# Kernel optimization log

Measured on AMD Instinct MI355X. Metric: run time of the kernel, lower is better.

Reference implementation:

```python
import jax, jax.numpy as jnp
import numpy as np

B, S, D = 1, 2048, 2048
H, HD = 32, 64            # num_heads, head_dim = hidden/num_heads
CS, TOPK = 256, 4         # moba_chunk_size, moba_topk
ROPE_BASE = 10000.0
EPS = 1e-6


def setup_inputs() -> dict:
    key = jax.random.key(0)
    ks = jax.random.split(key, 8)
    w = lambda k, shape: jax.random.normal(k, shape, dtype=jnp.float32) * 0.02
    return {
        "hidden_states": jax.random.normal(ks[0], (B, S, D), dtype=jnp.float32),
        "Wq": w(ks[1], (D, D)),
        "Wk": w(ks[2], (D, D)),
        "Wv": w(ks[3], (D, D)),
        "Wo": w(ks[4], (D, D)),
        "Wg1": w(ks[5], (D, HD)),
        "Wg2": w(ks[6], (HD, D)),
        "o_norm_w": jnp.ones((HD,), dtype=jnp.float32),
    }


def _rope(x):
    # x: [B,S,H,HD]; non-interleaved half-rotation rotary over full head_dim
    s = x.shape[1]
    half = HD // 2
    inv = 1.0 / (ROPE_BASE ** (jnp.arange(half, dtype=jnp.float32) / half))
    freqs = jnp.arange(s, dtype=jnp.float32)[:, None] * inv[None, :]      # [S, half]
    cos = jnp.cos(freqs)[None, :, None, :]
    sin = jnp.sin(freqs)[None, :, None, :]
    x1, x2 = x[..., :half], x[..., half:]
    return jnp.concatenate([x1 * cos - x2 * sin, x2 * cos + x1 * sin], axis=-1)


def _moba_attn_single(q, k, v):
    # q,k,v: [S,H,HD]  (one varlen sequence)
    s = q.shape[0]
    n = s // CS                                  # number of KV chunks
    scale = HD ** -0.5
    # mean-pooled key per chunk -> gate logits
    kg = k.reshape(n, CS, H, HD).mean(axis=1)                    # [N,H,HD]
    gate = jnp.einsum('shd,nhd->hsn', q, kg)                     # [H,S,N]
    pos_chunk = jnp.arange(s) // CS                              # [S]
    n_idx = jnp.arange(n)
    is_self = pos_chunk[:, None] == n_idx[None, :]               # [S,N]
    not_past = pos_chunk[:, None] <= n_idx[None, :]              # self or future
    gate = jnp.where(not_past[None], -jnp.inf, gate)             # only strictly-past chunks selectable
    gate = jnp.where(is_self[None], jnp.inf, gate)               # self chunk always attended
    kk = min(TOPK, n)
    tv, ti = jax.lax.top_k(gate, kk)                             # [H,S,kk], sorted desc
    thr = tv[..., -1:]                                           # min of top-k
    need = gate >= thr
    idx_mask = jax.nn.one_hot(ti, n, dtype=jnp.bool_).any(axis=-2)  # [H,S,N]
    need = need & idx_mask                                       # selected chunks per (h, query)
    # expand chunk selection to per-key mask and add causal mask
    allow = need[:, :, pos_chunk]                                # [H,S,S]
    causal = jnp.arange(s)[None, :] <= jnp.arange(s)[:, None]    # [S,S]
    mask = allow & causal[None]
    scores = jnp.einsum('shd,thd->hst', q, k) * scale            # [H,S,S]
    p = jax.nn.softmax(jnp.where(mask, scores, -jnp.inf), axis=-1)
    return jnp.einsum('hst,thd->shd', p, v)                      # [S,H,HD]


def reference(hidden_states, Wq, Wk, Wv, Wo, Wg1, Wg2, o_norm_w):
    x = hidden_states
    q = (x @ Wq).reshape(B, S, H, HD)
    k = (x @ Wk).reshape(B, S, H, HD)
    v = (x @ Wv).reshape(B, S, H, HD)
    q, k = _rope(q), _rope(k)
    o = jax.vmap(_moba_attn_single)(q, k, v)                     # [B,S,H,HD]
    # FusedRMSNormGated(sigmoid): rmsnorm(o) * weight * sigmoid(g)
    g = ((x @ Wg1) @ Wg2).reshape(B, S, H, HD)
    var = jnp.mean(o * o, axis=-1, keepdims=True)
    o = o * jax.lax.rsqrt(var + EPS) * o_norm_w
    o = o * jax.nn.sigmoid(g)
    return o.reshape(B, S, D) @ Wo
```

## Files before the change

kernel.cpp:

```cpp
#include <hip/hip_runtime.h>
#include <hip/hip_bf16.h>
#include <math.h>

#define S_LEN 2048
#define D_DIM 2048
#define NH 32
#define HD 64
#define CS 256
#define NCH 8

typedef __attribute__((ext_vector_type(8))) short bf16x8;
typedef __attribute__((ext_vector_type(4))) short bf16x4;
typedef __attribute__((ext_vector_type(4))) float f32x4;

__device__ __forceinline__ unsigned short f2bf(float f) {
  unsigned int u = __builtin_bit_cast(unsigned int, f);
  unsigned int r = (u + 0x7fffu + ((u >> 16) & 1u)) >> 16;
  return (unsigned short)r;
}
__device__ __forceinline__ float bf2f(unsigned short b) {
  unsigned int u = ((unsigned int)b) << 16;
  return __builtin_bit_cast(float, u);
}

__device__ __forceinline__ f32x4 mfma16(bf16x4 a, bf16x4 b, f32x4 c) {
#if __has_builtin(__builtin_amdgcn_mfma_f32_16x16x16_bf16)
  return __builtin_amdgcn_mfma_f32_16x16x16_bf16(a, b, c, 0, 0, 0);
#elif __has_builtin(__builtin_amdgcn_mfma_f32_16x16x16bf16_1k)
  return __builtin_amdgcn_mfma_f32_16x16x16bf16_1k(a, b, c, 0, 0, 0);
#else
  asm("v_mfma_f32_16x16x16_bf16 %0, %1, %2, %0" : "+v"(c) : "v"(a), "v"(b));
  return c;
#endif
}

__device__ __forceinline__ void gload16(const void* gp, void* lp) {
  __builtin_amdgcn_global_load_lds(
      (const __attribute__((address_space(1))) unsigned int*)gp,
      (__attribute__((address_space(3))) unsigned int*)lp, 16, 0, 0);
}

struct QKVG {
  const unsigned short* xh;
  const unsigned short* xl;
  const unsigned short* wh[4];
  const unsigned short* wl[4];
  float* C[4];
  int np[4];
};

__global__ __launch_bounds__(256) void gemm_qkvg(QKVG g) {
  __shared__ __align__(16) unsigned short Als[128 * 64];
  __shared__ __align__(16) unsigned short Bls[128 * 64];
  const int tid = threadIdx.x;
  const int wid = tid >> 6, lane = tid & 63;
  const int l15 = lane & 15, l4 = lane >> 4;
  const int wr = wid >> 1, wc = wid & 1;
  const int K = D_DIM, N = D_DIM;

  const int bid = blockIdx.x;
  const int xcd = bid & 7;
  const int local = bid >> 3;
  const int c = local >> 6;
  const int idx = local & 63;
  const int out = (xcd & 1) + 2 * c;
  const int grp = xcd >> 1;
  const int row0 = (idx >> 2) << 7;
  const int col0 = ((grp << 2) + (idx & 3)) << 7;

  f32x4 acc[4][4];
#pragma unroll
  for (int m = 0; m < 4; ++m)
#pragma unroll
    for (int n = 0; n < 4; ++n) acc[m][n] = (f32x4){0.f, 0.f, 0.f, 0.f};

  const int np = g.np[out];
  for (int p = 0; p < np; ++p) {
    const unsigned short* Ap = (p == 2) ? g.xl : g.xh;
    const unsigned short* Bp = (p == 1) ? g.wl[out] : g.wh[out];
    for (int kt = 0; kt < K; kt += 64) {
      __syncthreads();
#pragma unroll
      for (int i = 0; i < 4; ++i) {
        const int Lb = i * 4096 + wid * 1024;
        const int L = Lb + lane * 16;
        const int row = L >> 7;
        const int s = (L >> 4) & 7;
        const int cofs = (s ^ (row & 7)) << 3;
        gload16(Ap + (size_t)(row0 + row) * K + kt + cofs, (char*)Als + Lb);
        gload16(Bp + (size_t)(col0 + row) * K + kt + cofs, (char*)Bls + Lb);
      }
      asm volatile("s_waitcnt vmcnt(0)" ::: "memory");
      __syncthreads();
#pragma unroll
      for (int ks = 0; ks < 2; ++ks) {
        bf16x8 af[4], bfr[4];
#pragma unroll
        for (int m = 0; m < 4; ++m) {
          int row = wr * 64 + m * 16 + l15;
          int s = (ks * 4 + l4) ^ (row & 7);
          af[m] = *reinterpret_cast<const bf16x8*>(&Als[row * 64 + s * 8]);
        }
#pragma unroll
        for (int n = 0; n < 4; ++n) {
          int col = wc * 64 + n * 16 + l15;
          int s = (ks * 4 + l4) ^ (col & 7);
          bfr[n] = *reinterpret_cast<const bf16x8*>(&Bls[col * 64 + s * 8]);
        }
#pragma unroll
        for (int m = 0; m < 4; ++m)
#pragma unroll
          for (int n = 0; n < 4; ++n)
            acc[m][n] = __builtin_amdgcn_mfma_f32_16x16x32_bf16(af[m], bfr[n], acc[m][n], 0, 0, 0);
      }
    }
  }

  float* C = g.C[out];
#pragma unroll
  for (int m = 0; m < 4; ++m)
#pragma unroll
    for (int n = 0; n < 4; ++n)
#pragma unroll
      for (int r = 0; r < 4; ++r)
        C[(size_t)(row0 + wr * 64 + m * 16 + l4 * 4 + r) * N + col0 + wc * 64 + n * 16 + l15] =
            acc[m][n][r];
}

struct G3 {
  const unsigned short* A[3];
  const unsigned short* B[3];
  int np;
};

__global__ __launch_bounds__(256) void gemm_bt(G3 g, float* __restrict__ C,
                                               int M, int N, int K) {
  __shared__ __align__(16) unsigned short Als[64 * 64];
  __shared__ __align__(16) unsigned short Bls[128 * 64];
  const int tid = threadIdx.x;
  const int wid = tid >> 6, lane = tid & 63;
  const int l15 = lane & 15, l4 = lane >> 4;
  const int wr = wid >> 1, wc = wid & 1;
  const int nbx = N >> 7;
  int bid = blockIdx.x;
  const int nwg = gridDim.x;
  if ((nwg & 7) == 0) {
    int q = nwg >> 3;
    bid = (bid & 7) * q + (bid >> 3);
  }
  const int row0 = (bid / nbx) << 6;
  const int col0 = (bid % nbx) << 7;

  f32x4 acc[2][4];
#pragma unroll
  for (int m = 0; m < 2; ++m)
#pragma unroll
    for (int n = 0; n < 4; ++n) acc[m][n] = (f32x4){0.f, 0.f, 0.f, 0.f};

  for (int p = 0; p < g.np; ++p) {
    const unsigned short* Ap = g.A[p];
    const unsigned short* Bp = g.B[p];
    for (int kt = 0; kt < K; kt += 64) {
      __syncthreads();
#pragma unroll
      for (int i = 0; i < 2; ++i) {
        const int Lb = i * 4096 + wid * 1024;
        const int L = Lb + lane * 16;
        const int row = L >> 7;
        const int s = (L >> 4) & 7;
        const int cofs = (s ^ (row & 7)) << 3;
        gload16(Ap + (size_t)(row0 + row) * K + kt + cofs, (char*)Als + Lb);
      }
#pragma unroll
      for (int i = 0; i < 4; ++i) {
        const int Lb = i * 4096 + wid * 1024;
        const int L = Lb + lane * 16;
        const int row = L >> 7;
        const int s = (L >> 4) & 7;
        const int cofs = (s ^ (row & 7)) << 3;
        gload16(Bp + (size_t)(col0 + row) * K + kt + cofs, (char*)Bls + Lb);
      }
      asm volatile("s_waitcnt vmcnt(0)" ::: "memory");
      __syncthreads();
#pragma unroll
      for (int ks = 0; ks < 2; ++ks) {
        bf16x8 af[2], bfr[4];
#pragma unroll
        for (int m = 0; m < 2; ++m) {
          int row = wr * 32 + m * 16 + l15;
          int s = (ks * 4 + l4) ^ (row & 7);
          af[m] = *reinterpret_cast<const bf16x8*>(&Als[row * 64 + s * 8]);
        }
#pragma unroll
        for (int n = 0; n < 4; ++n) {
          int col = wc * 64 + n * 16 + l15;
          int s = (ks * 4 + l4) ^ (col & 7);
          bfr[n] = *reinterpret_cast<const bf16x8*>(&Bls[col * 64 + s * 8]);
        }
#pragma unroll
        for (int m = 0; m < 2; ++m)
#pragma unroll
          for (int n = 0; n < 4; ++n)
            acc[m][n] = __builtin_amdgcn_mfma_f32_16x16x32_bf16(af[m], bfr[n], acc[m][n], 0, 0, 0);
      }
    }
  }

#pragma unroll
  for (int m = 0; m < 2; ++m)
#pragma unroll
    for (int n = 0; n < 4; ++n)
#pragma unroll
      for (int r = 0; r < 4; ++r)
        C[(size_t)(row0 + wr * 32 + m * 16 + l4 * 4 + r) * N + col0 + wc * 64 + n * 16 + l15] =
            acc[m][n][r];
}

__global__ __launch_bounds__(256) void sgemm_f32(const float* __restrict__ A,
                                                 const float* __restrict__ B,
                                                 float* __restrict__ C,
                                                 int M, int N, int K) {
  __shared__ float As[8][128];
  __shared__ float Bs[8][128];
  const int tid = threadIdx.x;
  const int row0 = blockIdx.y * 128;
  const int col0 = blockIdx.x * 128;
  const int tm = (tid / 16) * 8;
  const int tn = (tid % 16) * 8;
  const int arow = tid >> 1;
  const int acol = (tid & 1) * 4;
  const int brow = tid >> 5;
  const int bcol = (tid & 31) * 4;

  float acc[8][8];
#pragma unroll
  for (int i = 0; i < 8; ++i)
#pragma unroll
    for (int j = 0; j < 8; ++j) acc[i][j] = 0.f;

  for (int k0 = 0; k0 < K; k0 += 8) {
    float4 av = make_float4(0.f, 0.f, 0.f, 0.f);
    if (row0 + arow < M) {
      int kb = k0 + acol;
      av = *reinterpret_cast<const float4*>(&A[(size_t)(row0 + arow) * K + kb]);
    }
    As[acol + 0][arow] = av.x;
    As[acol + 1][arow] = av.y;
    As[acol + 2][arow] = av.z;
    As[acol + 3][arow] = av.w;
    float4 bv = make_float4(0.f, 0.f, 0.f, 0.f);
    if (k0 + brow < K) {
      bv = *reinterpret_cast<const float4*>(&B[(size_t)(k0 + brow) * N + col0 + bcol]);
    }
    *reinterpret_cast<float4*>(&Bs[brow][bcol]) = bv;
    __syncthreads();
#pragma unroll
    for (int kk = 0; kk < 8; ++kk) {
      float a[8], b[8];
      *reinterpret_cast<float4*>(&a[0]) = *reinterpret_cast<const float4*>(&As[kk][tm]);
      *reinterpret_cast<float4*>(&a[4]) = *reinterpret_cast<const float4*>(&As[kk][tm + 4]);
      *reinterpret_cast<float4*>(&b[0]) = *reinterpret_cast<const float4*>(&Bs[kk][tn]);
      *reinterpret_cast<float4*>(&b[4]) = *reinterpret_cast<const float4*>(&Bs[kk][tn + 4]);
#pragma unroll
      for (int i = 0; i < 8; ++i)
#pragma unroll
        for (int j = 0; j < 8; ++j) acc[i][j] = fmaf(a[i], b[j], acc[i][j]);
    }
    __syncthreads();
  }
#pragma unroll
  for (int i = 0; i < 8; ++i) {
    int r = row0 + tm + i;
    if (r < M) {
#pragma unroll
      for (int j = 0; j < 8; ++j) {
        int c = col0 + tn + j;
        if (c < N) C[(size_t)r * N + c] = acc[i][j];
      }
    }
  }
}

__global__ __launch_bounds__(256) void repack_x_hl(const float* __restrict__ x,
                                                   unsigned short* __restrict__ xh,
                                                   unsigned short* __restrict__ xl) {
  int i = (blockIdx.x * 256 + threadIdx.x) * 4;
  float4 v = *reinterpret_cast<const float4*>(&x[i]);
  float f[4] = {v.x, v.y, v.z, v.w};
  unsigned short h[4], l[4];
#pragma unroll
  for (int j = 0; j < 4; ++j) {
    h[j] = f2bf(f[j]);
    l[j] = f2bf(f[j] - bf2f(h[j]));
  }
  *reinterpret_cast<ushort4*>(&xh[i]) = make_ushort4(h[0], h[1], h[2], h[3]);
  *reinterpret_cast<ushort4*>(&xl[i]) = make_ushort4(l[0], l[1], l[2], l[3]);
}

__global__ __launch_bounds__(256) void repack_T(const float* __restrict__ W,
                                                unsigned short* __restrict__ hiT,
                                                unsigned short* __restrict__ loT,
                                                int rows, int cols, int has_lo) {
  __shared__ float t[64][65];
  const int k0 = blockIdx.y * 64, n0 = blockIdx.x * 64;
  const int tid = threadIdx.x;
  const int c = tid & 63, rr = tid >> 6;
#pragma unroll
  for (int r = 0; r < 16; ++r) {
    int kr = r * 4 + rr;
    t[kr][c] = W[(size_t)(k0 + kr) * cols + n0 + c];
  }
  __syncthreads();
#pragma unroll
  for (int r = 0; r < 16; ++r) {
    int n = r * 4 + rr;
    float f = t[c][n];
    unsigned short hb = f2bf(f);
    hiT[(size_t)(n0 + n) * rows + k0 + c] = hb;
    if (has_lo) loT[(size_t)(n0 + n) * rows + k0 + c] = f2bf(f - bf2f(hb));
  }
}

struct RT3 {
  const float* W[3];
  unsigned short* hiT[3];
  unsigned short* loT[3];
  int has_lo[3];
};

__global__ __launch_bounds__(256) void repack_T3(RT3 a) {
  __shared__ float t[64][65];
  const int wsel = blockIdx.z;
  const float* W = a.W[wsel];
  unsigned short* hiT = a.hiT[wsel];
  unsigned short* loT = a.loT[wsel];
  const int has_lo = a.has_lo[wsel];
  const int k0 = blockIdx.y * 64, n0 = blockIdx.x * 64;
  const int tid = threadIdx.x;
  const int c = tid & 63, rr = tid >> 6;
#pragma unroll
  for (int r = 0; r < 16; ++r) {
    int kr = r * 4 + rr;
    t[kr][c] = W[(size_t)(k0 + kr) * D_DIM + n0 + c];
  }
  __syncthreads();
#pragma unroll
  for (int r = 0; r < 16; ++r) {
    int n = r * 4 + rr;
    float f = t[c][n];
    unsigned short hb = f2bf(f);
    hiT[(size_t)(n0 + n) * D_DIM + k0 + c] = hb;
    if (has_lo) loT[(size_t)(n0 + n) * D_DIM + k0 + c] = f2bf(f - bf2f(hb));
  }
}

__global__ __launch_bounds__(256) void rope_qk(float* __restrict__ q, float* __restrict__ kk) {
  int idx = blockIdx.x * 256 + threadIdx.x;
  if (idx >= S_LEN * NH * (HD / 2)) return;
  int d = idx & 31;
  int sh = idx >> 5;
  int s = sh >> 5;
  float inv = 1.0f / powf(10000.0f, (float)d * (1.0f / 32.0f));
  float fr = (float)s * inv;
  float c = cosf(fr), sn = sinf(fr);
  size_t base = (size_t)sh * HD + d;
  float q1 = q[base], q2 = q[base + 32];
  q[base] = q1 * c - q2 * sn;
  q[base + 32] = q2 * c + q1 * sn;
  float k1 = kk[base], k2 = kk[base + 32];
  kk[base] = k1 * c - k2 * sn;
  kk[base + 32] = k2 * c + k1 * sn;
}

__global__ __launch_bounds__(256) void chunk_mean(const float* __restrict__ k,
                                                  float* __restrict__ kg) {
  int idx = blockIdx.x * 256 + threadIdx.x;
  if (idx >= NCH * NH * HD) return;
  int c = idx / (NH * HD);
  int hd = idx % (NH * HD);
  float sum = 0.f;
  for (int t = 0; t < CS; ++t) sum += k[(size_t)(c * CS + t) * (NH * HD) + hd];
  kg[idx] = sum * (1.0f / CS);
}

__global__ __launch_bounds__(256) void gate_topk(const float* __restrict__ q,
                                                 const float* __restrict__ kg,
                                                 int* __restrict__ amask) {
  int wid = threadIdx.x >> 6;
  int lane = threadIdx.x & 63;
  int s = blockIdx.x * 4 + wid;
  int h = blockIdx.y;
  int myc = s >> 8;
  float qd = q[((size_t)s * NH + h) * HD + lane];
  float g[NCH];
#pragma unroll
  for (int c = 0; c < NCH; ++c) {
    float p = qd * kg[((size_t)c * NH + h) * HD + lane];
#pragma unroll
    for (int off = 32; off; off >>= 1) p += __shfl_xor(p, off);
    g[c] = p;
  }
  int chosen = 0;
#pragma unroll
  for (int pick = 0; pick < 3; ++pick) {
    float best = -INFINITY;
    int bi = -1;
#pragma unroll
    for (int c = 0; c < NCH; ++c) {
      if (c < myc && !((chosen >> c) & 1) && g[c] > best) {
        best = g[c];
        bi = c;
      }
    }
    if (bi >= 0) chosen |= (1 << bi);
  }
  int mask = chosen | (1 << myc);
  if (lane == 0) amask[h * S_LEN + s] = mask;
}

__global__ __launch_bounds__(256) void repack_kf(const float* __restrict__ k,
                                                 unsigned short* __restrict__ khf) {
  __shared__ float tl[64][68];
  const int t = blockIdx.x;
  const int h = blockIdx.y;
  const int tid = threadIdx.x;
  const int t0 = t * 64;
  {
    const int r = tid >> 2, c4 = (tid & 3) * 16;
    const float* src = &k[((size_t)(t0 + r) * NH + h) * HD + c4];
#pragma unroll
    for (int qd = 0; qd < 4; ++qd)
      *reinterpret_cast<float4*>(&tl[r][c4 + qd * 4]) =
          *reinterpret_cast<const float4*>(src + qd * 4);
  }
  __syncthreads();
  const int w = tid >> 6, l = tid & 63;
  const int l15 = l & 15, g = l >> 4;
  unsigned short* ob = khf + (((size_t)h * 32 + t) * 8) * 512;
#pragma unroll
  for (int ff = 0; ff < 2; ++ff) {
    const int f = 2 * w + ff;
    const int st = f >> 1, half = f & 1;
    const float* rp = &tl[st * 16 + l15][g * 8 + half * 32];
    ushort4 u0 = make_ushort4(f2bf(rp[0]), f2bf(rp[1]), f2bf(rp[2]), f2bf(rp[3]));
    ushort4 u1 = make_ushort4(f2bf(rp[4]), f2bf(rp[5]), f2bf(rp[6]), f2bf(rp[7]));
    *reinterpret_cast<ushort4*>(ob + (size_t)f * 512 + l * 8) = u0;
    *reinterpret_cast<ushort4*>(ob + (size_t)f * 512 + l * 8 + 4) = u1;
  }
}

__global__ __launch_bounds__(256) void repack_vf(const float* __restrict__ v,
                                                 unsigned short* __restrict__ vhf) {
  __shared__ float tl[64][68];
  const int t = blockIdx.x;
  const int h = blockIdx.y;
  const int tid = threadIdx.x;
  const int t0 = t * 64;
  {
    const int r = tid >> 2, c4 = (tid & 3) * 16;
    const float* src = &v[((size_t)(t0 + r) * NH + h) * HD + c4];
#pragma unroll
    for (int qd = 0; qd < 4; ++qd)
      *reinterpret_cast<float4*>(&tl[r][c4 + qd * 4]) =
          *reinterpret_cast<const float4*>(src + qd * 4);
  }
  __syncthreads();
  const int w = tid >> 6, l = tid & 63;
  const int l15 = l & 15, g = l >> 4;
  unsigned short* ob = vhf + (((size_t)h * 32 + t) * 8) * 512;
#pragma unroll
  for (int ff = 0; ff < 2; ++ff) {
    const int fp = 2 * w + ff;
    const int st = fp >> 1, p = fp & 1;
    unsigned short u[8];
#pragma unroll
    for (int e = 0; e < 8; ++e) {
      const int cb = 2 * p + (e >> 2);
      const int j = e & 3;
      u[e] = f2bf(tl[st * 16 + 4 * g + j][cb * 16 + l15]);
    }
    *reinterpret_cast<ushort4*>(ob + (size_t)fp * 512 + l * 8) =
        make_ushort4(u[0], u[1], u[2], u[3]);
    *reinterpret_cast<ushort4*>(ob + (size_t)fp * 512 + l * 8 + 4) =
        make_ushort4(u[4], u[5], u[6], u[7]);
  }
}

__global__ __launch_bounds__(256) void attn_mfma(const float* __restrict__ q,
                                                 const unsigned short* __restrict__ khf,
                                                 const unsigned short* __restrict__ vhf,
                                                 const int* __restrict__ amask,
                                                 float* __restrict__ o) {
  const int B = blockIdx.x;
  const int xcd = B & 7;
  const int jb = B >> 3;
  const int h = xcd + ((jb >> 7) << 3);
  const int s0 = (jb & 127) << 4;
  const int tid = threadIdx.x;
  const int wid = tid >> 6;
  const int lane = tid & 63;
  const int l15 = lane & 15, g = lane >> 4;
  const int myS = s0 + l15;
  const int myc = s0 >> 8;
  const int ktm = (s0 & (CS - 1)) >> 6;

  __shared__ float lm[4][16];
  __shared__ float ll[4][16];
  __shared__ float lacc[4][16][64];

  const float* qrow = q + ((size_t)myS * NH + h) * HD;
  bf16x8 qf[2];
#pragma unroll
  for (int hf = 0; hf < 2; ++hf)
#pragma unroll
    for (int jj = 0; jj < 8; ++jj)
      qf[hf][jj] = (short)f2bf(qrow[hf * 32 + g * 8 + jj] * 0.125f);

  int mymask = amask[h * S_LEN + myS];
  int wmask = mymask;
  wmask |= __shfl_xor(wmask, 1);
  wmask |= __shfl_xor(wmask, 2);
  wmask |= __shfl_xor(wmask, 4);
  wmask |= __shfl_xor(wmask, 8);
  const int pmask = wmask & ~(1 << myc);
  const int ntot = (ktm + 1) + 4 * __popc(pmask);

  auto DEC = [&](int j) -> int {
    if (j <= ktm) return ((s0 & ~255) + (j << 6)) | (1 << 16);
    int jj = j - ktm - 1;
    int mm = pmask;
    int drop = jj >> 2;
    for (int b = 0; b < drop; ++b) mm &= mm - 1;
    int c = __ffs(mm) - 1;
    return ((c << 8) + ((jj & 3) << 6)) | (((mymask >> c) & 1) << 16);
  };

  const unsigned short* khh = khf + (((size_t)h * 32) << 12);
  const unsigned short* vhh = vhf + (((size_t)h * 32) << 12);

  bf16x8 kr[4][2];
  auto LOADK = [&](int t0) {
    const unsigned short* tb = khh + ((size_t)(t0 >> 6) << 12) + lane * 8;
#pragma unroll
    for (int f = 0; f < 8; ++f)
      kr[f >> 1][f & 1] = *reinterpret_cast<const bf16x8*>(tb + f * 512);
  };

  float m = -1e30f, lsum = 0.f;
  f32x4 accv[4];
#pragma unroll
  for (int i = 0; i < 4; ++i) accv[i] = (f32x4){0.f, 0.f, 0.f, 0.f};

  if (wid < ntot) LOADK(DEC(wid) & 0xFFFF);

#pragma unroll
  for (int i = 0; i < 8; ++i) {
    const int j = wid + (i << 2);
    if (j < ntot) {
      const int ent = DEC(j);
      const int t0 = ent & 0xFFFF;
      const bool lane_on = (ent >> 16) != 0;
      const bool diag = (j == ktm);

      const unsigned short* vtb = vhh + ((size_t)(t0 >> 6) << 12) + lane * 8;
      bf16x4 vb[4][4];
#pragma unroll
      for (int fp = 0; fp < 8; ++fp) {
        bf16x8 wv = *reinterpret_cast<const bf16x8*>(vtb + fp * 512);
        const int st = fp >> 1, pp = fp & 1;
#pragma unroll
        for (int jj = 0; jj < 4; ++jj) {
          vb[st][2 * pp][jj] = wv[jj];
          vb[st][2 * pp + 1][jj] = wv[4 + jj];
        }
      }

      float p[16];
      __builtin_amdgcn_s_setprio(1);
#pragma unroll
      for (int st = 0; st < 4; ++st) {
        f32x4 d = (f32x4){0.f, 0.f, 0.f, 0.f};
        d = __builtin_amdgcn_mfma_f32_16x16x32_bf16(kr[st][0], qf[0], d, 0, 0, 0);
        d = __builtin_amdgcn_mfma_f32_16x16x32_bf16(kr[st][1], qf[1], d, 0, 0, 0);
#pragma unroll
        for (int r = 0; r < 4; ++r) {
          bool ok = lane_on && (!diag || (t0 + st * 16 + 4 * g + r <= myS));
          p[st * 4 + r] = ok ? d[r] : -1e30f;
        }
      }
      __builtin_amdgcn_s_setprio(0);

      if (j + 4 < ntot) LOADK(DEC(j + 4) & 0xFFFF);

      float mt = -1e30f;
#pragma unroll
      for (int ii = 0; ii < 16; ++ii) mt = fmaxf(mt, p[ii]);
      mt = fmaxf(mt, __shfl_xor(mt, 16));
      mt = fmaxf(mt, __shfl_xor(mt, 32));

      const float mnew = fmaxf(m, mt);
      const float corr = __expf(m - mnew);
      float ps = 0.f;
#pragma unroll
      for (int ii = 0; ii < 16; ++ii) {
        float pv = (p[ii] > -1e29f) ? __expf(p[ii] - mnew) : 0.f;
        p[ii] = pv;
        ps += pv;
      }
      ps += __shfl_xor(ps, 16);
      ps += __shfl_xor(ps, 32);
      lsum = lsum * corr + ps;
      m = mnew;

#pragma unroll
      for (int r = 0; r < 4; ++r) {
        float cr = __shfl(corr, 4 * g + r);
#pragma unroll
        for (int cb = 0; cb < 4; ++cb) accv[cb][r] *= cr;
      }

      __builtin_amdgcn_s_setprio(1);
#pragma unroll
      for (int st = 0; st < 4; ++st) {
        bf16x4 pa;
#pragma unroll
        for (int jj = 0; jj < 4; ++jj) pa[jj] = (short)f2bf(p[st * 4 + jj]);
#pragma unroll
        for (int cb = 0; cb < 4; ++cb)
          accv[cb] = mfma16(pa, vb[st][cb], accv[cb]);
      }
      __builtin_amdgcn_s_setprio(0);
    }
  }

#pragma unroll
  for (int cb = 0; cb < 4; ++cb)
#pragma unroll
    for (int r = 0; r < 4; ++r) lacc[wid][cb * 4 + r][lane] = accv[cb][r];
  if (lane < 16) {
    lm[wid][lane] = m;
    ll[wid][lane] = lsum;
  }
  __syncthreads();

  float outv[4];
#pragma unroll
  for (int r = 0; r < 4; ++r) {
    const int row = 4 * g + r;
    float m0 = lm[0][row], m1 = lm[1][row], m2 = lm[2][row], m3 = lm[3][row];
    float mt = fmaxf(fmaxf(m0, m1), fmaxf(m2, m3));
    float e0 = __expf(m0 - mt), e1 = __expf(m1 - mt);
    float e2 = __expf(m2 - mt), e3 = __expf(m3 - mt);
    float ltot = ll[0][row] * e0 + ll[1][row] * e1 + ll[2][row] * e2 + ll[3][row] * e3;
    float a = lacc[0][wid * 4 + r][lane] * e0 + lacc[1][wid * 4 + r][lane] * e1 +
              lacc[2][wid * 4 + r][lane] * e2 + lacc[3][wid * 4 + r][lane] * e3;
    outv[r] = a / ltot;
  }
#pragma unroll
  for (int r = 0; r < 4; ++r)
    o[((size_t)(s0 + 4 * g + r) * NH + h) * HD + wid * 16 + l15] = outv[r];
}

__global__ __launch_bounds__(256) void postproc(const float* __restrict__ o,
                                                const float* __restrict__ g,
                                                const float* __restrict__ w,
                                                unsigned short* __restrict__ o2h) {
  int idx = blockIdx.x * 256 + threadIdx.x;
  int lane = threadIdx.x & 63;
  float val = o[idx];
  float ss = val * val;
#pragma unroll
  for (int off = 32; off; off >>= 1) ss += __shfl_xor(ss, off);
  float r = rsqrtf(ss * (1.0f / HD) + 1e-6f);
  float gv = g[idx];
  float sig = 1.0f / (1.0f + expf(-gv));
  o2h[idx] = f2bf(val * r * w[lane] * sig);
}

extern "C" void kernel_launch(void* const* d_in, const int* in_sizes, int n_in,
                              void* d_out, int out_size, void* d_ws, size_t ws_size,
                              hipStream_t stream) {
  const float* x   = (const float*)d_in[0];
  const float* Wq  = (const float*)d_in[1];
  const float* Wk  = (const float*)d_in[2];
  const float* Wv  = (const float*)d_in[3];
  const float* Wo  = (const float*)d_in[4];
  const float* Wg1 = (const float*)d_in[5];
  const float* Wg2 = (const float*)d_in[6];
  const float* onw = (const float*)d_in[7];
  float* out = (float*)d_out;

  const size_t BIG = (size_t)S_LEN * D_DIM;
  float* q    = (float*)d_ws;
  float* k    = q + BIG;
  float* v    = k + BIG;
  float* o    = v + BIG;
  float* gbuf = o + BIG;
  float* kg   = gbuf + BIG;
  int* amask  = (int*)(kg + NCH * NH * HD);
  unsigned short* xh  = (unsigned short*)(amask + NH * S_LEN);
  unsigned short* xl  = xh + BIG;
  unsigned short* whq = xl + BIG;
  unsigned short* wlq = whq + BIG;
  unsigned short* whk = wlq + BIG;
  unsigned short* wlk = whk + BIG;
  unsigned short* whv = wlk + BIG;
  unsigned short* whg = whv + BIG;
  unsigned short* khf = whg + BIG;
  unsigned short* vhf = khf + BIG;
  unsigned short* o2h = vhf + BIG;

  const dim3 gT(32, 32);
  repack_x_hl<<<(int)(BIG / 4 / 256), 256, 0, stream>>>(x, xh, xl);
  {
    RT3 rt;
    rt.W[0] = Wq;  rt.hiT[0] = whq; rt.loT[0] = wlq; rt.has_lo[0] = 1;
    rt.W[1] = Wk;  rt.hiT[1] = whk; rt.loT[1] = wlk; rt.has_lo[1] = 1;
    rt.W[2] = Wv;  rt.hiT[2] = whv; rt.loT[2] = whv; rt.has_lo[2] = 0;
    repack_T3<<<dim3(32, 32, 3), 256, 0, stream>>>(rt);
  }
  sgemm_f32<<<dim3(16, 16), 256, 0, stream>>>(Wg1, Wg2, o, D_DIM, D_DIM, HD);
  repack_T<<<gT, 256, 0, stream>>>(o, whg, nullptr, D_DIM, D_DIM, 0);

  {
    QKVG gg;
    gg.xh = xh; gg.xl = xl;
    gg.wh[0] = whq; gg.wh[1] = whk; gg.wh[2] = whv; gg.wh[3] = whg;
    gg.wl[0] = wlq; gg.wl[1] = wlk; gg.wl[2] = nullptr; gg.wl[3] = nullptr;
    gg.C[0] = q; gg.C[1] = k; gg.C[2] = v; gg.C[3] = gbuf;
    gg.np[0] = 3; gg.np[1] = 3; gg.np[2] = 1; gg.np[3] = 1;
    gemm_qkvg<<<1024, 256, 0, stream>>>(gg);
  }

  rope_qk<<<S_LEN * NH * (HD / 2) / 256, 256, 0, stream>>>(q, k);
  chunk_mean<<<(NCH * NH * HD + 255) / 256, 256, 0, stream>>>(k, kg);
  gate_topk<<<dim3(S_LEN / 4, NH), 256, 0, stream>>>(q, kg, amask);
  repack_kf<<<dim3(S_LEN / 64, NH), 256, 0, stream>>>(k, khf);
  repack_vf<<<dim3(S_LEN / 64, NH), 256, 0, stream>>>(v, vhf);
  attn_mfma<<<(S_LEN / 16) * NH, 256, 0, stream>>>(q, khf, vhf, amask, o);
  postproc<<<(int)(BIG / 256), 256, 0, stream>>>(o, gbuf, onw, o2h);
  repack_T<<<gT, 256, 0, stream>>>(Wo, whq, nullptr, D_DIM, D_DIM, 0);
  {
    G3 g3{{o2h, o2h, o2h}, {whq, whq, whq}, 1};
    gemm_bt<<<(S_LEN / 64) * (D_DIM / 128), 256, 0, stream>>>(g3, out, S_LEN, D_DIM, D_DIM);
  }
}
```

Baseline: 370.5 us.

## Fuse RoPE into QKV GEMM epilogue and merge repack/postproc kernels

Applies rotary embedding inside the QKV GEMM epilogue using a precomputed cos/sin table, which removes the separate in-place RoPE pass over q and k. The Wg1·Wg2 product is written directly as a transposed bf16 operand, dropping one f32 buffer round-trip and a transpose kernel. The Wo transpose moves into the batched repack, and the K and V repacks become one kernel. Postproc is vectorised to four elements per thread. Together these cut kernel launches and global memory traffic, at the cost of a small table kernel and extra epilogue work in the GEMM.

```diff
diff --git a/kernel.cpp b/kernel.cpp
--- a/kernel.cpp
+++ b/kernel.cpp
@@ -40,6 +40,16 @@
       (__attribute__((address_space(3))) unsigned int*)lp, 16, 0, 0);
 }
 
+__global__ __launch_bounds__(256) void rope_tab_k(float2* __restrict__ tab) {
+  int idx = blockIdx.x * 256 + threadIdx.x;
+  if (idx >= S_LEN * 32) return;
+  int d = idx & 31;
+  int s = idx >> 5;
+  float inv = 1.0f / powf(10000.0f, (float)d * (1.0f / 32.0f));
+  float fr = (float)s * inv;
+  tab[idx] = make_float2(cosf(fr), sinf(fr));
+}
+
 struct QKVG {
   const unsigned short* xh;
   const unsigned short* xl;
@@ -47,6 +57,7 @@
   const unsigned short* wl[4];
   float* C[4];
   int np[4];
+  const float2* rtab;
 };
 
 __global__ __launch_bounds__(256) void gemm_qkvg(QKVG g) {
@@ -113,6 +124,23 @@
           for (int n = 0; n < 4; ++n)
             acc[m][n] = __builtin_amdgcn_mfma_f32_16x16x32_bf16(af[m], bfr[n], acc[m][n], 0, 0, 0);
       }
+    }
+  }
+
+  if (out < 2) {
+#pragma unroll
+    for (int n = 0; n < 2; ++n) {
+      const int d = n * 16 + l15;
+#pragma unroll
+      for (int m = 0; m < 4; ++m)
+#pragma unroll
+        for (int r = 0; r < 4; ++r) {
+          const int s = row0 + wr * 64 + m * 16 + l4 * 4 + r;
+          float2 cs = g.rtab[s * 32 + d];
+          float a1 = acc[m][n][r], a2 = acc[m][n + 2][r];
+          acc[m][n][r] = a1 * cs.x - a2 * cs.y;
+          acc[m][n + 2][r] = a2 * cs.x + a1 * cs.y;
+        }
     }
   }
 
@@ -216,10 +244,10 @@
             acc[m][n][r];
 }
 
-__global__ __launch_bounds__(256) void sgemm_f32(const float* __restrict__ A,
-                                                 const float* __restrict__ B,
-                                                 float* __restrict__ C,
-                                                 int M, int N, int K) {
+__global__ __launch_bounds__(256) void sgemm_f32T(const float* __restrict__ A,
+                                                  const float* __restrict__ B,
+                                                  unsigned short* __restrict__ CT,
+                                                  int M, int N, int K) {
   __shared__ float As[8][128];
   __shared__ float Bs[8][128];
   const int tid = threadIdx.x;
@@ -269,15 +297,12 @@
     __syncthreads();
   }
 #pragma unroll
-  for (int i = 0; i < 8; ++i) {
-    int r = row0 + tm + i;
-    if (r < M) {
-#pragma unroll
-      for (int j = 0; j < 8; ++j) {
-        int c = col0 + tn + j;
-        if (c < N) C[(size_t)r * N + c] = acc[i][j];
-      }
-    }
+  for (int j = 0; j < 8; ++j) {
+    const int n = col0 + tn + j;
+    ushort4 u0 = make_ushort4(f2bf(acc[0][j]), f2bf(acc[1][j]), f2bf(acc[2][j]), f2bf(acc[3][j]));
+    ushort4 u1 = make_ushort4(f2bf(acc[4][j]), f2bf(acc[5][j]), f2bf(acc[6][j]), f2bf(acc[7][j]));
+    *reinterpret_cast<ushort4*>(&CT[(size_t)n * M + row0 + tm]) = u0;
+    *reinterpret_cast<ushort4*>(&CT[(size_t)n * M + row0 + tm + 4]) = u1;
   }
 }
 
@@ -297,38 +322,14 @@
   *reinterpret_cast<ushort4*>(&xl[i]) = make_ushort4(l[0], l[1], l[2], l[3]);
 }
 
-__global__ __launch_bounds__(256) void repack_T(const float* __restrict__ W,
-                                                unsigned short* __restrict__ hiT,
-                                                unsigned short* __restrict__ loT,
-                                                int rows, int cols, int has_lo) {
-  __shared__ float t[64][65];
-  const int k0 = blockIdx.y * 64, n0 = blockIdx.x * 64;
-  const int tid = threadIdx.x;
-  const int c = tid & 63, rr = tid >> 6;
-#pragma unroll
-  for (int r = 0; r < 16; ++r) {
-    int kr = r * 4 + rr;
-    t[kr][c] = W[(size_t)(k0 + kr) * cols + n0 + c];
-  }
-  __syncthreads();
-#pragma unroll
-  for (int r = 0; r < 16; ++r) {
-    int n = r * 4 + rr;
-    float f = t[c][n];
-    unsigned short hb = f2bf(f);
-    hiT[(size_t)(n0 + n) * rows + k0 + c] = hb;
-    if (has_lo) loT[(size_t)(n0 + n) * rows + k0 + c] = f2bf(f - bf2f(hb));
-  }
-}
-
-struct RT3 {
-  const float* W[3];
-  unsigned short* hiT[3];
-  unsigned short* loT[3];
-  int has_lo[3];
+struct RT4 {
+  const float* W[4];
+  unsigned short* hiT[4];
+  unsigned short* loT[4];
+  int has_lo[4];
 };
 
-__global__ __launch_bounds__(256) void repack_T3(RT3 a) {
+__global__ __launch_bounds__(256) void repack_T4(RT4 a) {
   __shared__ float t[64][65];
   const int wsel = blockIdx.z;
   const float* W = a.W[wsel];
@@ -352,24 +353,6 @@
     hiT[(size_t)(n0 + n) * D_DIM + k0 + c] = hb;
     if (has_lo) loT[(size_t)(n0 + n) * D_DIM + k0 + c] = f2bf(f - bf2f(hb));
   }
-}
-
-__global__ __launch_bounds__(256) void rope_qk(float* __restrict__ q, float* __restrict__ kk) {
-  int idx = blockIdx.x * 256 + threadIdx.x;
-  if (idx >= S_LEN * NH * (HD / 2)) return;
-  int d = idx & 31;
-  int sh = idx >> 5;
-  int s = sh >> 5;
-  float inv = 1.0f / powf(10000.0f, (float)d * (1.0f / 32.0f));
-  float fr = (float)s * inv;
-  float c = cosf(fr), sn = sinf(fr);
-  size_t base = (size_t)sh * HD + d;
-  float q1 = q[base], q2 = q[base + 32];
-  q[base] = q1 * c - q2 * sn;
-  q[base + 32] = q2 * c + q1 * sn;
-  float k1 = kk[base], k2 = kk[base + 32];
-  kk[base] = k1 * c - k2 * sn;
-  kk[base + 32] = k2 * c + k1 * sn;
 }
 
 __global__ __launch_bounds__(256) void chunk_mean(const float* __restrict__ k,
@@ -418,71 +401,58 @@
   if (lane == 0) amask[h * S_LEN + s] = mask;
 }
 
-__global__ __launch_bounds__(256) void repack_kf(const float* __restrict__ k,
-                                                 unsigned short* __restrict__ khf) {
-  __shared__ float tl[64][68];
+__global__ __launch_bounds__(256) void repack_kvf(const float* __restrict__ k,
+                                                  const float* __restrict__ v,
+                                                  unsigned short* __restrict__ khf,
+                                                  unsigned short* __restrict__ vhf) {
+  __shared__ float tk[64][68];
+  __shared__ float tv[64][68];
   const int t = blockIdx.x;
   const int h = blockIdx.y;
   const int tid = threadIdx.x;
   const int t0 = t * 64;
   {
     const int r = tid >> 2, c4 = (tid & 3) * 16;
-    const float* src = &k[((size_t)(t0 + r) * NH + h) * HD + c4];
-#pragma unroll
-    for (int qd = 0; qd < 4; ++qd)
-      *reinterpret_cast<float4*>(&tl[r][c4 + qd * 4]) =
-          *reinterpret_cast<const float4*>(src + qd * 4);
+    const float* sk = &k[((size_t)(t0 + r) * NH + h) * HD + c4];
+    const float* sv = &v[((size_t)(t0 + r) * NH + h) * HD + c4];
+#pragma unroll
+    for (int qd = 0; qd < 4; ++qd) {
+      *reinterpret_cast<float4*>(&tk[r][c4 + qd * 4]) =
+          *reinterpret_cast<const float4*>(sk + qd * 4);
+      *reinterpret_cast<float4*>(&tv[r][c4 + qd * 4]) =
+          *reinterpret_cast<const float4*>(sv + qd * 4);
+    }
   }
   __syncthreads();
   const int w = tid >> 6, l = tid & 63;
   const int l15 = l & 15, g = l >> 4;
-  unsigned short* ob = khf + (((size_t)h * 32 + t) * 8) * 512;
+  unsigned short* obk = khf + (((size_t)h * 32 + t) * 8) * 512;
+  unsigned short* obv = vhf + (((size_t)h * 32 + t) * 8) * 512;
 #pragma unroll
   for (int ff = 0; ff < 2; ++ff) {
     const int f = 2 * w + ff;
-    const int st = f >> 1, half = f & 1;
-    const float* rp = &tl[st * 16 + l15][g * 8 + half * 32];
-    ushort4 u0 = make_ushort4(f2bf(rp[0]), f2bf(rp[1]), f2bf(rp[2]), f2bf(rp[3]));
-    ushort4 u1 = make_ushort4(f2bf(rp[4]), f2bf(rp[5]), f2bf(rp[6]), f2bf(rp[7]));
-    *reinterpret_cast<ushort4*>(ob + (size_t)f * 512 + l * 8) = u0;
-    *reinterpret_cast<ushort4*>(ob + (size_t)f * 512 + l * 8 + 4) = u1;
-  }
-}
-
-__global__ __launch_bounds__(256) void repack_vf(const float* __restrict__ v,
-                                                 unsigned short* __restrict__ vhf) {
-  __shared__ float tl[64][68];
-  const int t = blockIdx.x;
-  const int h = blockIdx.y;
-  const int tid = threadIdx.x;
-  const int t0 = t * 64;
-  {
-    const int r = tid >> 2, c4 = (tid & 3) * 16;
-    const float* src = &v[((size_t)(t0 + r) * NH + h) * HD + c4];
-#pragma unroll
-    for (int qd = 0; qd < 4; ++qd)
-      *reinterpret_cast<float4*>(&tl[r][c4 + qd * 4]) =
-          *reinterpret_cast<const float4*>(src + qd * 4);
-  }
-  __syncthreads();
-  const int w = tid >> 6, l = tid & 63;
-  const int l15 = l & 15, g = l >> 4;
-  unsigned short* ob = vhf + (((size_t)h * 32 + t) * 8) * 512;
-#pragma unroll
-  for (int ff = 0; ff < 2; ++ff) {
-    const int fp = 2 * w + ff;
-    const int st = fp >> 1, p = fp & 1;
-    unsigned short u[8];
-#pragma unroll
-    for (int e = 0; e < 8; ++e) {
-      const int cb = 2 * p + (e >> 2);
-      const int j = e & 3;
-      u[e] = f2bf(tl[st * 16 + 4 * g + j][cb * 16 + l15]);
-    }
-    *reinterpret_cast<ushort4*>(ob + (size_t)fp * 512 + l * 8) =
-        make_ushort4(u[0], u[1], u[2], u[3]);
-    *reinterpret_cast<ushort4*>(ob + (size_t)fp * 512 + l * 8 + 4) =
-        make_ushort4(u[4], u[5], u[6], u[7]);
+    {
+      const int st = f >> 1, half = f & 1;
+      const float* rp = &tk[st * 16 + l15][g * 8 + half * 32];
+      ushort4 u0 = make_ushort4(f2bf(rp[0]), f2bf(rp[1]), f2bf(rp[2]), f2bf(rp[3]));
+      ushort4 u1 = make_ushort4(f2bf(rp[4]), f2bf(rp[5]), f2bf(rp[6]), f2bf(rp[7]));
+      *reinterpret_cast<ushort4*>(obk + (size_t)f * 512 + l * 8) = u0;
+      *reinterpret_cast<ushort4*>(obk + (size_t)f * 512 + l * 8 + 4) = u1;
+    }
+    {
+      const int st = f >> 1, p = f & 1;
+      unsigned short u[8];
+#pragma unroll
+      for (int e = 0; e < 8; ++e) {
+        const int cb = 2 * p + (e >> 2);
+        const int j = e & 3;
+        u[e] = f2bf(tv[st * 16 + 4 * g + j][cb * 16 + l15]);
+      }
+      *reinterpret_cast<ushort4*>(obv + (size_t)f * 512 + l * 8) =
+          make_ushort4(u[0], u[1], u[2], u[3]);
+      *reinterpret_cast<ushort4*>(obv + (size_t)f * 512 + l * 8 + 4) =
+          make_ushort4(u[4], u[5], u[6], u[7]);
+    }
   }
 }
 
@@ -665,16 +635,23 @@
                                                 const float* __restrict__ g,
                                                 const float* __restrict__ w,
                                                 unsigned short* __restrict__ o2h) {
-  int idx = blockIdx.x * 256 + threadIdx.x;
-  int lane = threadIdx.x & 63;
-  float val = o[idx];
-  float ss = val * val;
-#pragma unroll
-  for (int off = 32; off; off >>= 1) ss += __shfl_xor(ss, off);
+  int base = (blockIdx.x * 256 + threadIdx.x) * 4;
+  int l16 = threadIdx.x & 15;
+  float4 val = *reinterpret_cast<const float4*>(&o[base]);
+  float ss = val.x * val.x + val.y * val.y + val.z * val.z + val.w * val.w;
+#pragma unroll
+  for (int off = 1; off < 16; off <<= 1) ss += __shfl_xor(ss, off);
   float r = rsqrtf(ss * (1.0f / HD) + 1e-6f);
-  float gv = g[idx];
-  float sig = 1.0f / (1.0f + expf(-gv));
-  o2h[idx] = f2bf(val * r * w[lane] * sig);
+  float4 gv = *reinterpret_cast<const float4*>(&g[base]);
+  float f[4] = {val.x, val.y, val.z, val.w};
+  float gg[4] = {gv.x, gv.y, gv.z, gv.w};
+  unsigned short u[4];
+#pragma unroll
+  for (int j = 0; j < 4; ++j) {
+    float sig = 1.0f / (1.0f + expf(-gg[j]));
+    u[j] = f2bf(f[j] * r * w[l16 * 4 + j] * sig);
+  }
+  *reinterpret_cast<ushort4*>(&o2h[base]) = make_ushort4(u[0], u[1], u[2], u[3]);
 }
 
 extern "C" void kernel_launch(void* const* d_in, const int* in_sizes, int n_in,
@@ -698,7 +675,8 @@
   float* gbuf = o + BIG;
   float* kg   = gbuf + BIG;
   int* amask  = (int*)(kg + NCH * NH * HD);
-  unsigned short* xh  = (unsigned short*)(amask + NH * S_LEN);
+  float2* rtab = (float2*)(amask + NH * S_LEN);
+  unsigned short* xh  = (unsigned short*)(rtab + S_LEN * 32);
   unsigned short* xl  = xh + BIG;
   unsigned short* whq = xl + BIG;
   unsigned short* wlq = whq + BIG;
@@ -706,21 +684,22 @@
   unsigned short* wlk = whk + BIG;
   unsigned short* whv = wlk + BIG;
   unsigned short* whg = whv + BIG;
-  unsigned short* khf = whg + BIG;
+  unsigned short* who = whg + BIG;
+  unsigned short* khf = who + BIG;
   unsigned short* vhf = khf + BIG;
   unsigned short* o2h = vhf + BIG;
 
-  const dim3 gT(32, 32);
+  rope_tab_k<<<(S_LEN * 32 + 255) / 256, 256, 0, stream>>>(rtab);
   repack_x_hl<<<(int)(BIG / 4 / 256), 256, 0, stream>>>(x, xh, xl);
   {
-    RT3 rt;
-    rt.W[0] = Wq;  rt.hiT[0] = whq; rt.loT[0] = wlq; rt.has_lo[0] = 1;
-    rt.W[1] = Wk;  rt.hiT[1] = whk; rt.loT[1] = wlk; rt.has_lo[1] = 1;
-    rt.W[2] = Wv;  rt.hiT[2] = whv; rt.loT[2] = whv; rt.has_lo[2] = 0;
-    repack_T3<<<dim3(32, 32, 3), 256, 0, stream>>>(rt);
-  }
-  sgemm_f32<<<dim3(16, 16), 256, 0, stream>>>(Wg1, Wg2, o, D_DIM, D_DIM, HD);
-  repack_T<<<gT, 256, 0, stream>>>(o, whg, nullptr, D_DIM, D_DIM, 0);
+    RT4 rt;
+    rt.W[0] = Wq; rt.hiT[0] = whq; rt.loT[0] = wlq; rt.has_lo[0] = 1;
+    rt.W[1] = Wk; rt.hiT[1] = whk; rt.loT[1] = wlk; rt.has_lo[1] = 1;
+    rt.W[2] = Wv; rt.hiT[2] = whv; rt.loT[2] = whv; rt.has_lo[2] = 0;
+    rt.W[3] = Wo; rt.hiT[3] = who; rt.loT[3] = who; rt.has_lo[3] = 0;
+    repack_T4<<<dim3(32, 32, 4), 256, 0, stream>>>(rt);
+  }
+  sgemm_f32T<<<dim3(16, 16), 256, 0, stream>>>(Wg1, Wg2, whg, D_DIM, D_DIM, HD);
 
   {
     QKVG gg;
@@ -729,19 +708,17 @@
     gg.wl[0] = wlq; gg.wl[1] = wlk; gg.wl[2] = nullptr; gg.wl[3] = nullptr;
     gg.C[0] = q; gg.C[1] = k; gg.C[2] = v; gg.C[3] = gbuf;
     gg.np[0] = 3; gg.np[1] = 3; gg.np[2] = 1; gg.np[3] = 1;
+    gg.rtab = rtab;
     gemm_qkvg<<<1024, 256, 0, stream>>>(gg);
   }
 
-  rope_qk<<<S_LEN * NH * (HD / 2) / 256, 256, 0, stream>>>(q, k);
   chunk_mean<<<(NCH * NH * HD + 255) / 256, 256, 0, stream>>>(k, kg);
   gate_topk<<<dim3(S_LEN / 4, NH), 256, 0, stream>>>(q, kg, amask);
-  repack_kf<<<dim3(S_LEN / 64, NH), 256, 0, stream>>>(k, khf);
-  repack_vf<<<dim3(S_LEN / 64, NH), 256, 0, stream>>>(v, vhf);
+  repack_kvf<<<dim3(S_LEN / 64, NH), 256, 0, stream>>>(k, v, khf, vhf);
   attn_mfma<<<(S_LEN / 16) * NH, 256, 0, stream>>>(q, khf, vhf, amask, o);
-  postproc<<<(int)(BIG / 256), 256, 0, stream>>>(o, gbuf, onw, o2h);
-  repack_T<<<gT, 256, 0, stream>>>(Wo, whq, nullptr, D_DIM, D_DIM, 0);
+  postproc<<<(int)(BIG / 4 / 256), 256, 0, stream>>>(o, gbuf, onw, o2h);
   {
-    G3 g3{{o2h, o2h, o2h}, {whq, whq, whq}, 1};
+    G3 g3{{o2h, o2h, o2h}, {who, who, who}, 1};
     gemm_bt<<<(S_LEN / 64) * (D_DIM / 128), 256, 0, stream>>>(g3, out, S_LEN, D_DIM, D_DIM);
   }
 }
```

Result: faster. 343.3 us (-7.3%).
